# Kernel tuning notes

Measured on AMD Instinct MI355X. Metric: run time of the kernel, lower is better.

Reference implementation:

```python
import jax, jax.numpy as jnp
import numpy as np
from jax import lax

B, T1, T2, D, H = 4, 1024, 1024, 1024, 16
DK = D // H          # 64 per-head dim
K = 13               # conv kernel size
FF = 4 * D


def _ln(x, g, b, eps):
    mu = jnp.mean(x, axis=-1, keepdims=True)
    var = jnp.mean((x - mu) ** 2, axis=-1, keepdims=True)
    y = (x - mu) * lax.rsqrt(var + eps)
    if g is not None:
        y = y * g + b
    return y


def _conv1d(x, w, b):
    # x: (B, T, C) ; w: (O, C//H, K) grouped conv, 'same' padding
    y = lax.conv_general_dilated(
        x.transpose(0, 2, 1), w, window_strides=(1,),
        padding=[(K // 2, K // 2)],
        dimension_numbers=('NCH', 'OIH', 'NCH'),
        feature_group_count=H)
    return (y + b[None, :, None]).transpose(0, 2, 1)


def setup_inputs() -> dict:
    key = jax.random.key(0)
    ks = jax.random.split(key, 24)
    s = 0.02
    inp = {
        'noisy_feats': jax.random.normal(ks[0], (B, T1, D), jnp.float32),
        'clean_feats': jax.random.normal(ks[1], (B, T2, D), jnp.float32),
        't': jax.random.normal(ks[2], (B, D), jnp.float32),
        'ln_noisy_g': jnp.ones((D,), jnp.float32),
        'ln_noisy_b': jnp.zeros((D,), jnp.float32),
        'ln_clean_g': jnp.ones((D,), jnp.float32),
        'ln_clean_b': jnp.zeros((D,), jnp.float32),
        'ada_w': jax.random.normal(ks[3], (6 * D, D), jnp.float32) * s,
        'ada_b': jnp.zeros((6 * D,), jnp.float32),
        'wq': jax.random.normal(ks[4], (D, D // H, K), jnp.float32) * s,
        'bq': jnp.zeros((D,), jnp.float32),
        'wk': jax.random.normal(ks[5], (D, D // H, K), jnp.float32) * s,
        'bk': jnp.zeros((D,), jnp.float32),
        'wv': jax.random.normal(ks[6], (D, D // H, K), jnp.float32) * s,
        'bv': jnp.zeros((D,), jnp.float32),
        'fc_w': jax.random.normal(ks[7], (D, D), jnp.float32) * s,
        'fc_b': jnp.zeros((D,), jnp.float32),
        'ff_w1': jax.random.normal(ks[8], (FF, D), jnp.float32) * s,
        'ff_b1': jnp.zeros((FF,), jnp.float32),
        'ff_w2': jax.random.normal(ks[9], (D, FF), jnp.float32) * s,
        'ff_b2': jnp.zeros((D,), jnp.float32),
        'noisy_lengths': jax.random.randint(ks[10], (B,), 1, T1 + 1),
        'clean_lengths': jax.random.randint(ks[11], (B,), 1, T2 + 1),
    }
    return inp


def reference(noisy_feats, clean_feats, t,
              ln_noisy_g, ln_noisy_b, ln_clean_g, ln_clean_b,
              ada_w, ada_b, wq, bq, wk, bk, wv, bv, fc_w, fc_b,
              ff_w1, ff_b1, ff_w2, ff_b2,
              noisy_lengths, clean_lengths):
    # pre-norms (affine, eps=1e-5 torch default)
    noisy = _ln(noisy_feats, ln_noisy_g, ln_noisy_b, 1e-5)
    clean = _ln(clean_feats, ln_clean_g, ln_clean_b, 1e-5)

    # AdaLayerNormZero
    emb = jax.nn.silu(t) @ ada_w.T + ada_b                      # (B, 6D)
    shift_msa, scale_msa, gate_msa, shift_mlp, scale_mlp, gate_mlp = jnp.split(emb, 6, axis=1)
    normx = _ln(noisy, None, None, 1e-6) * (1.0 + scale_msa[:, None]) + shift_msa[:, None]

    # padding mask: True at pad positions (only context mask enters the scores)
    clean_mask = jnp.arange(T2)[None, :] >= clean_lengths[:, None]   # (B, T2)

    # grouped-conv QKV
    q = _conv1d(normx, wq, bq).reshape(B, T1, H, DK)
    k = _conv1d(clean, wk, bk).reshape(B, T2, H, DK)
    v = _conv1d(clean, wv, bv).reshape(B, T2, H, DK)

    scores = jnp.einsum('bqhd,bkhd->bhqk', q, k) / jnp.sqrt(jnp.float32(DK))
    scores = jnp.where(clean_mask[:, None, None, :], jnp.float32(-1e30), scores)
    p = jax.nn.softmax(scores, axis=-1)
    # rows where every key is masked -> zero (torch all_inf handling)
    all_masked = jnp.all(clean_mask, axis=-1)[:, None, None, None]
    p = jnp.where(all_masked, 0.0, p)

    out = jnp.einsum('bhqk,bkhd->bqhd', p, v).reshape(B, T1, D)
    out = out @ fc_w.T + fc_b

    x = noisy + gate_msa[:, None, :] * out
    n2 = _ln(x, None, None, 1e-6) * (1.0 + scale_mlp[:, None]) + shift_mlp[:, None]
    ff = jax.nn.gelu(n2 @ ff_w1.T + ff_b1, approximate=True) @ ff_w2.T + ff_b2
    return x + gate_mlp[:, None, :] * ff
```

## Files before the change

### kernel.cpp

```cpp
#include <hip/hip_runtime.h>
#include <hip/hip_bf16.h>

typedef __hip_bfloat16 bf16;
typedef __attribute__((ext_vector_type(8))) short short8;
typedef __attribute__((ext_vector_type(4))) float f32x4;

#define D_ 1024
#define SIXD 6144

__device__ __forceinline__ float bflo(unsigned int u){ union {unsigned int u; float f;} c; c.u = u << 16; return c.f; }
__device__ __forceinline__ float bfhi(unsigned int u){ union {unsigned int u; float f;} c; c.u = u & 0xFFFF0000u; return c.f; }
__device__ __forceinline__ float bload(const bf16* p){
  union {unsigned int u; float f;} c;
  c.u = ((unsigned int)(*reinterpret_cast<const unsigned short*>(p))) << 16;
  return c.f;
}
__device__ __forceinline__ bf16 bstore(float f){ return __float2bfloat16(f); }
__device__ __forceinline__ unsigned short bf16bits(float f){
  bf16 b = __float2bfloat16(f);
  return *reinterpret_cast<unsigned short*>(&b);
}

__device__ __forceinline__ void gload16(const bf16* g, bf16* l){
  __builtin_amdgcn_global_load_lds((const __attribute__((address_space(1))) unsigned int*)g,
                                   (__attribute__((address_space(3))) unsigned int*)l, 16, 0, 0);
}

__device__ __forceinline__ void pipe_sync(){
  asm volatile("s_waitcnt vmcnt(0)" ::: "memory");
  __builtin_amdgcn_s_barrier();
  __builtin_amdgcn_sched_barrier(0);
}

template<int ISBF>
__device__ __forceinline__ float ild(const void* p, size_t i){
  if (ISBF) return bload((const bf16*)p + i);
  return ((const float*)p)[i];
}

__device__ __forceinline__ float block_sum(float v, float* sh4){
  #pragma unroll
  for (int o = 32; o; o >>= 1) v += __shfl_down(v, o);
  __syncthreads();
  int lane = threadIdx.x & 63, wid = threadIdx.x >> 6;
  if (lane == 0) sh4[wid] = v;
  __syncthreads();
  return sh4[0] + sh4[1] + sh4[2] + sh4[3];
}

__global__ void detect_kernel(const unsigned int* g, int* flag){
  unsigned int u = *g;
  *flag = (u == 0x3F803F80u) ? 1 : 0;
}

template<int ISBF>
__device__ __forceinline__ void emb_body(const void* T, const void* AW, const void* AB,
                                         float* E, float* st){
  int b = blockIdx.y;
  int tid = threadIdx.x;
  for (int c = tid; c < D_; c += 256) {
    float x = ild<ISBF>(T, (size_t)b*D_ + c);
    st[c] = x / (1.f + expf(-x));
  }
  __syncthreads();
  int wid = tid >> 6, lane = tid & 63;
  int j = blockIdx.x * 4 + wid;
  float dot = 0.f;
  for (int c = lane; c < D_; c += 64) dot += ild<ISBF>(AW, (size_t)j*D_ + c) * st[c];
  #pragma unroll
  for (int o = 32; o; o >>= 1) dot += __shfl_down(dot, o);
  if (lane == 0) E[b*SIXD + j] = dot + ild<ISBF>(AB, j);
}
__global__ __launch_bounds__(256) void emb_kernel(const void* T, const void* AW, const void* AB,
                                                  const int* flagp, float* E){
  __shared__ float st[D_];
  if (*flagp) emb_body<1>(T, AW, AB, E, st); else emb_body<0>(T, AW, AB, E, st);
}

template<int ISBF>
__device__ __forceinline__ void ln_noisy_body(const void* X, const void* G, const void* Bt,
                                              const float* E, bf16* xbuf, bf16* normx, float* sh4){
  int r = blockIdx.x; int b = r >> 10;
  int tid = threadIdx.x; int c0 = tid * 4;
  size_t base = (size_t)r*D_ + c0;
  float f0 = ild<ISBF>(X, base+0), f1 = ild<ISBF>(X, base+1);
  float f2 = ild<ISBF>(X, base+2), f3 = ild<ISBF>(X, base+3);
  float mean = block_sum(f0+f1+f2+f3, sh4) * (1.f/D_);
  float var  = block_sum(f0*f0+f1*f1+f2*f2+f3*f3, sh4) * (1.f/D_) - mean*mean;
  float rstd = rsqrtf(fmaxf(var, 0.f) + 1e-5f);
  float y0 = (f0-mean)*rstd*ild<ISBF>(G,c0+0) + ild<ISBF>(Bt,c0+0);
  float y1 = (f1-mean)*rstd*ild<ISBF>(G,c0+1) + ild<ISBF>(Bt,c0+1);
  float y2 = (f2-mean)*rstd*ild<ISBF>(G,c0+2) + ild<ISBF>(Bt,c0+2);
  float y3 = (f3-mean)*rstd*ild<ISBF>(G,c0+3) + ild<ISBF>(Bt,c0+3);
  bf16* xo = xbuf + base;
  xo[0]=bstore(y0); xo[1]=bstore(y1); xo[2]=bstore(y2); xo[3]=bstore(y3);
  float m2 = block_sum(y0+y1+y2+y3, sh4) * (1.f/D_);
  float v2 = block_sum(y0*y0+y1*y1+y2*y2+y3*y3, sh4) * (1.f/D_) - m2*m2;
  float rstd2 = rsqrtf(fmaxf(v2, 0.f) + 1e-6f);
  const float* eb = E + b*SIXD;
  bf16* o = normx + base;
  o[0] = bstore((y0-m2)*rstd2*(1.f+eb[1024+c0+0]) + eb[c0+0]);
  o[1] = bstore((y1-m2)*rstd2*(1.f+eb[1024+c0+1]) + eb[c0+1]);
  o[2] = bstore((y2-m2)*rstd2*(1.f+eb[1024+c0+2]) + eb[c0+2]);
  o[3] = bstore((y3-m2)*rstd2*(1.f+eb[1024+c0+3]) + eb[c0+3]);
}
__global__ __launch_bounds__(256) void ln_noisy_fused(const void* X, const void* G, const void* Bt,
                                                      const float* E, bf16* xbuf, bf16* normx,
                                                      const int* flagp){
  __shared__ float sh4[4];
  if (*flagp) ln_noisy_body<1>(X,G,Bt,E,xbuf,normx,sh4); else ln_noisy_body<0>(X,G,Bt,E,xbuf,normx,sh4);
}

template<int ISBF>
__device__ __forceinline__ void ln_clean_body(const void* X, const void* G, const void* Bt,
                                              bf16* Y, float* sh4){
  int r = blockIdx.x;
  int tid = threadIdx.x; int c0 = tid * 4;
  size_t base = (size_t)r*D_ + c0;
  float f0 = ild<ISBF>(X, base+0), f1 = ild<ISBF>(X, base+1);
  float f2 = ild<ISBF>(X, base+2), f3 = ild<ISBF>(X, base+3);
  float mean = block_sum(f0+f1+f2+f3, sh4) * (1.f/D_);
  float var  = block_sum(f0*f0+f1*f1+f2*f2+f3*f3, sh4) * (1.f/D_) - mean*mean;
  float rstd = rsqrtf(fmaxf(var, 0.f) + 1e-5f);
  bf16* o = Y + base;
  o[0] = bstore((f0-mean)*rstd*ild<ISBF>(G,c0+0) + ild<ISBF>(Bt,c0+0));
  o[1] = bstore((f1-mean)*rstd*ild<ISBF>(G,c0+1) + ild<ISBF>(Bt,c0+1));
  o[2] = bstore((f2-mean)*rstd*ild<ISBF>(G,c0+2) + ild<ISBF>(Bt,c0+2));
  o[3] = bstore((f3-mean)*rstd*ild<ISBF>(G,c0+3) + ild<ISBF>(Bt,c0+3));
}
__global__ __launch_bounds__(256) void ln_clean_kernel(const void* X, const void* G, const void* Bt,
                                                       bf16* Y, const int* flagp){
  __shared__ float sh4[4];
  if (*flagp) ln_clean_body<1>(X,G,Bt,Y,sh4); else ln_clean_body<0>(X,G,Bt,Y,sh4);
}

__global__ __launch_bounds__(256) void ln2_kernel(const bf16* __restrict__ X, const float* __restrict__ E,
                                                  bf16* __restrict__ Y){
  __shared__ float sh4[4];
  int r = blockIdx.x; int b = r >> 10;
  int tid = threadIdx.x; int c0 = tid * 4;
  uint2 u = *reinterpret_cast<const uint2*>(X + (size_t)r*D_ + c0);
  float f0 = bflo(u.x), f1 = bfhi(u.x), f2 = bflo(u.y), f3 = bfhi(u.y);
  float mean = block_sum(f0+f1+f2+f3, sh4) * (1.f/D_);
  float var  = block_sum(f0*f0+f1*f1+f2*f2+f3*f3, sh4) * (1.f/D_) - mean*mean;
  float rstd = rsqrtf(fmaxf(var, 0.f) + 1e-6f);
  const float* eb = E + b*SIXD;
  bf16* o = Y + (size_t)r*D_ + c0;
  o[0] = bstore((f0-mean)*rstd*(1.f+eb[4096+c0+0]) + eb[3072+c0+0]);
  o[1] = bstore((f1-mean)*rstd*(1.f+eb[4096+c0+1]) + eb[3072+c0+1]);
  o[2] = bstore((f2-mean)*rstd*(1.f+eb[4096+c0+2]) + eb[3072+c0+2]);
  o[3] = bstore((f3-mean)*rstd*(1.f+eb[4096+c0+3]) + eb[3072+c0+3]);
}

template<int ISBF>
__device__ __forceinline__ void wtrans_body(const void* W, bf16* Wtr){
  size_t idx = (size_t)blockIdx.x * 256 + threadIdx.x;
  int si = idx & 63;
  size_t r = idx >> 6;
  int o = (int)(r & 63); r >>= 6;
  int k = (int)(r % 13);
  int g = (int)(r / 13);
  int i = si ^ ((o & 7) << 3);
  Wtr[idx] = bstore(ild<ISBF>(W, ((size_t)(g*64 + o)*64 + i)*13 + k));
}
__global__ __launch_bounds__(256) void conv_wtrans(const void* W, bf16* Wtr, const int* flagp){
  if (*flagp) wtrans_body<1>(W, Wtr); else wtrans_body<0>(W, Wtr);
}

template<int ISBF>
__device__ __forceinline__ void wconv_body(const void* W, bf16* o, int n){
  for (int i = blockIdx.x*256 + threadIdx.x; i < n; i += gridDim.x*256)
    o[i] = bstore(ild<ISBF>(W, (size_t)i));
}
__global__ __launch_bounds__(256) void wconv_kernel(const void* W, bf16* o, int n, const int* flagp){
  if (*flagp) wconv_body<1>(W, o, n); else wconv_body<0>(W, o, n);
}

template<int ISBF>
__device__ __forceinline__ void convl_body(const bf16* __restrict__ X,
                                           const bf16* __restrict__ Wtr, const void* Bias,
                                           bf16* __restrict__ Y,
                                           bf16* ws, bf16* xs){
  int tid = threadIdx.x;
  int wave = tid >> 6, lane = tid & 63;
  int fr = lane & 15, fq = lane >> 4;
  int t0 = blockIdx.x * 256;
  int g = blockIdx.y, b = blockIdx.z;
  const bf16* Wg = Wtr + (size_t)g*53248;
  #pragma unroll
  for (int p = 0; p < 13; ++p)
    gload16(Wg + ((size_t)p*512 + tid)*8, ws + (p*512 + tid)*8);
  const bf16* xg = X + ((size_t)b*1024)*D_ + g*64;
  for (int idx = tid; idx < 268*8; idx += 512) {
    int row = idx >> 3, q = idx & 7;
    int t = t0 - 6 + row;
    uint4 v = make_uint4(0,0,0,0);
    if (t >= 0 && t < 1024)
      v = *reinterpret_cast<const uint4*>(xg + (size_t)t*D_ + q*8);
    *reinterpret_cast<uint4*>(&xs[row*72 + q*8]) = v;
  }
  __syncthreads();
  f32x4 acc[2][4];
  #pragma unroll
  for (int i = 0; i < 2; ++i)
    #pragma unroll
    for (int j = 0; j < 4; ++j) acc[i][j] = (f32x4){0.f,0.f,0.f,0.f};
  int wrow = wave * 32;
  const bf16* a0 = xs + (wrow + fr)*72 + fq*8;
  for (int k = 0; k < 13; ++k) {
    const bf16* wk_ = ws + (k*64 + fr)*64;
    const bf16* ar = a0 + k*72;
    #pragma unroll
    for (int h = 0; h < 2; ++h) {
      int swz = (h*32 + fq*8) ^ ((fr & 7) << 3);
      short8 af0 = *reinterpret_cast<const short8*>(ar + h*32);
      short8 af1 = *reinterpret_cast<const short8*>(ar + 16*72 + h*32);
      #pragma unroll
      for (int tn = 0; tn < 4; ++tn) {
        short8 bv = *reinterpret_cast<const short8*>(wk_ + tn*1024 + swz);
        acc[0][tn] = __builtin_amdgcn_mfma_f32_16x16x32_bf16(af0, bv, acc[0][tn], 0,0,0);
        acc[1][tn] = __builtin_amdgcn_mfma_f32_16x16x32_bf16(af1, bv, acc[1][tn], 0,0,0);
      }
    }
  }
  #pragma unroll
  for (int tm = 0; tm < 2; ++tm) {
    #pragma unroll
    for (int tn = 0; tn < 4; ++tn) {
      int oc = g*64 + tn*16 + fr;
      float bb = ild<ISBF>(Bias, oc);
      #pragma unroll
      for (int r = 0; r < 4; ++r) {
        int tt = t0 + wrow + tm*16 + fq*4 + r;
        Y[((size_t)(b*1024 + tt))*D_ + oc] = bstore(acc[tm][tn][r] + bb);
      }
    }
  }
}
__global__ __launch_bounds__(512) void conv_lds(const bf16* X, const bf16* Wtr, const void* Bias,
                                                bf16* Y, const int* flagp){
  extern __shared__ bf16 smem[];
  bf16* ws = smem;
  bf16* xs = smem + 53248;
  if (*flagp) convl_body<1>(X, Wtr, Bias, Y, ws, xs);
  else        convl_body<0>(X, Wtr, Bias, Y, ws, xs);
}
#define CONV_LDS_BYTES ((53248 + 268*72) * 2)

__global__ __launch_bounds__(256) void attn_mfma(const bf16* __restrict__ Q, const bf16* __restrict__ Kb,
                                                 const bf16* __restrict__ V, const int* __restrict__ lens,
                                                 bf16* __restrict__ O){
  __shared__ bf16 qs[64*72];
  __shared__ bf16 ks[64*72];
  __shared__ bf16 vt[64*72];
  __shared__ bf16 ps[4][16*72];
  int tid = threadIdx.x;
  int wave = tid >> 6, lane = tid & 63;
  int fr = lane & 15, fq = lane >> 4;
  int qb = blockIdx.x, h = blockIdx.y, b = blockIdx.z;
  int len = lens[b]; len = len < 0 ? 0 : (len > 1024 ? 1024 : len);
  {
    int row = tid >> 2, col = (tid & 3) * 16;
    const bf16* src = Q + ((size_t)(b*1024 + qb*64 + row))*D_ + h*64 + col;
    *reinterpret_cast<uint4*>(&qs[row*72 + col])     = *reinterpret_cast<const uint4*>(src);
    *reinterpret_cast<uint4*>(&qs[row*72 + col + 8]) = *reinterpret_cast<const uint4*>(src + 8);
  }
  __syncthreads();
  short8 bq0 = *reinterpret_cast<const short8*>(&qs[(wave*16 + fr)*72 + fq*8]);
  short8 bq1 = *reinterpret_cast<const short8*>(&qs[(wave*16 + fr)*72 + 32 + fq*8]);
  f32x4 oacc[4];
  #pragma unroll
  for (int t = 0; t < 4; ++t) oacc[t] = (f32x4){0.f,0.f,0.f,0.f};
  float m_ = -1e30f, l_ = 0.f;
  int krow = tid >> 2, kcol = (tid & 3) * 16;
  int vk = (tid >> 3) * 2, vcol = (tid & 7) * 8;
  const bf16* kg = Kb + ((size_t)b*1024)*D_ + h*64;
  const bf16* vg = V  + ((size_t)b*1024)*D_ + h*64;
  for (int k0 = 0; k0 < len; k0 += 64) {
    uint4 kv0 = make_uint4(0,0,0,0), kv1 = make_uint4(0,0,0,0);
    uint4 va = make_uint4(0,0,0,0), vb = make_uint4(0,0,0,0);
    if (k0 + krow < len) {
      kv0 = *reinterpret_cast<const uint4*>(kg + (size_t)(k0+krow)*D_ + kcol);
      kv1 = *reinterpret_cast<const uint4*>(kg + (size_t)(k0+krow)*D_ + kcol + 8);
    }
    if (k0 + vk < len)     va = *reinterpret_cast<const uint4*>(vg + (size_t)(k0+vk)*D_ + vcol);
    if (k0 + vk + 1 < len) vb = *reinterpret_cast<const uint4*>(vg + (size_t)(k0+vk+1)*D_ + vcol);
    __syncthreads();
    *reinterpret_cast<uint4*>(&ks[krow*72 + kcol])     = kv0;
    *reinterpret_cast<uint4*>(&ks[krow*72 + kcol + 8]) = kv1;
    {
      union { uint4 u; unsigned short s[8]; } ca, cb; ca.u = va; cb.u = vb;
      #pragma unroll
      for (int j = 0; j < 8; ++j) {
        unsigned int w = ((unsigned int)cb.s[j] << 16) | (unsigned int)ca.s[j];
        int d = vcol + j;
        int blk = ((vk >> 3) ^ ((d >> 3) & 7)) << 3;
        *reinterpret_cast<unsigned int*>(&vt[d*72 + blk + (vk & 7)]) = w;
      }
    }
    __syncthreads();
    f32x4 s[4];
    #pragma unroll
    for (int f = 0; f < 4; ++f) {
      short8 ak0 = *reinterpret_cast<const short8*>(&ks[(f*16 + fr)*72 + fq*8]);
      short8 ak1 = *reinterpret_cast<const short8*>(&ks[(f*16 + fr)*72 + 32 + fq*8]);
      s[f] = (f32x4){0.f,0.f,0.f,0.f};
      s[f] = __builtin_amdgcn_mfma_f32_16x16x32_bf16(ak0, bq0, s[f], 0,0,0);
      s[f] = __builtin_amdgcn_mfma_f32_16x16x32_bf16(ak1, bq1, s[f], 0,0,0);
    }
    float p[4][4];
    float pmax = -1e30f;
    #pragma unroll
    for (int f = 0; f < 4; ++f)
      #pragma unroll
      for (int r = 0; r < 4; ++r) {
        float sv = (k0 + f*16 + fq*4 + r < len) ? s[f][r]*0.125f : -1e30f;
        p[f][r] = sv;
        pmax = fmaxf(pmax, sv);
      }
    pmax = fmaxf(pmax, __shfl_xor(pmax, 16));
    pmax = fmaxf(pmax, __shfl_xor(pmax, 32));
    float mnew = fmaxf(m_, pmax);
    float alpha = __expf(m_ - mnew);
    float psum = 0.f;
    #pragma unroll
    for (int f = 0; f < 4; ++f)
      #pragma unroll
      for (int r = 0; r < 4; ++r) {
        float pv = __expf(p[f][r] - mnew);
        p[f][r] = pv;
        psum += pv;
      }
    psum += __shfl_xor(psum, 16);
    psum += __shfl_xor(psum, 32);
    l_ = l_*alpha + psum;
    m_ = mnew;
    #pragma unroll
    for (int f = 0; f < 4; ++f) {
      unsigned int lo = ((unsigned int)bf16bits(p[f][1]) << 16) | (unsigned int)bf16bits(p[f][0]);
      unsigned int hi = ((unsigned int)bf16bits(p[f][3]) << 16) | (unsigned int)bf16bits(p[f][2]);
      unsigned int* pp = reinterpret_cast<unsigned int*>(&ps[wave][fr*72 + f*16 + fq*4]);
      pp[0] = lo; pp[1] = hi;
    }
    float aq[4];
    #pragma unroll
    for (int r = 0; r < 4; ++r) aq[r] = __shfl(alpha, fq*4 + r);
    #pragma unroll
    for (int tn = 0; tn < 4; ++tn)
      #pragma unroll
      for (int r = 0; r < 4; ++r) oacc[tn][r] *= aq[r];
    short8 ap0 = *reinterpret_cast<const short8*>(&ps[wave][fr*72 + fq*8]);
    short8 ap1 = *reinterpret_cast<const short8*>(&ps[wave][fr*72 + 32 + fq*8]);
    #pragma unroll
    for (int tn = 0; tn < 4; ++tn) {
      int d = tn*16 + fr;
      int sw = (d >> 3) & 7;
      short8 bv0 = *reinterpret_cast<const short8*>(&vt[d*72 + ((fq     ^ sw) << 3)]);
      short8 bv1 = *reinterpret_cast<const short8*>(&vt[d*72 + (((4+fq) ^ sw) << 3)]);
      oacc[tn] = __builtin_amdgcn_mfma_f32_16x16x32_bf16(ap0, bv0, oacc[tn], 0,0,0);
      oacc[tn] = __builtin_amdgcn_mfma_f32_16x16x32_bf16(ap1, bv1, oacc[tn], 0,0,0);
    }
  }
  float linv = (l_ > 0.f) ? 1.f/l_ : 0.f;
  float iq[4];
  #pragma unroll
  for (int r = 0; r < 4; ++r) iq[r] = __shfl(linv, fq*4 + r);
  #pragma unroll
  for (int r = 0; r < 4; ++r) {
    int q = qb*64 + wave*16 + fq*4 + r;
    bf16* op = O + ((size_t)(b*1024 + q))*D_ + h*64 + fr;
    #pragma unroll
    for (int tn = 0; tn < 4; ++tn)
      op[tn*16] = bstore(oacc[tn][r] * iq[r]);
  }
}

template<int ISBF>
__device__ __forceinline__ void mgemm_body(const bf16* __restrict__ A, const bf16* __restrict__ W,
                                           const void* bias, int bofs,
                                           int K, int ldA, int ldW, int Nst, int mode, int gate_ofs,
                                           bf16* xbuf, const float* emb, void* outb,
                                           bf16* As, bf16* Bs){
  int tid = threadIdx.x;
  int nwg = gridDim.x * gridDim.y;
  int flat = blockIdx.y * gridDim.x + blockIdx.x;
  int swz = (flat & 7) * (nwg >> 3) + (flat >> 3);
  int bx = swz % gridDim.x, by = swz / gridDim.x;
  int m0 = by * 128, n0 = bx * 128;
  int wave = tid >> 6, lane = tid & 63;
  int wr = wave >> 2, wc = wave & 3;
  int fr = lane & 15, fq = lane >> 4;
  int srow = tid >> 2, skc = (tid & 3) * 8;
  const bf16* Ag = A + (size_t)(m0 + srow)*ldA + skc;
  const bf16* Wg = W + (size_t)(n0 + srow)*ldW + skc;
  bf16* Asl = As + tid*8;
  bf16* Bsl = Bs + tid*8;
  const bf16* Afr = As + (wr*64 + fr)*32 + fq*8;
  const bf16* Bfr = Bs + (wc*32 + fr)*32 + fq*8;
  f32x4 acc[4][2];
  #pragma unroll
  for (int i = 0; i < 4; ++i)
    #pragma unroll
    for (int j = 0; j < 2; ++j) acc[i][j] = (f32x4){0.f,0.f,0.f,0.f};
  gload16(Ag,      Asl);
  gload16(Ag + 32, Asl + 4096);
  gload16(Wg,      Bsl);
  gload16(Wg + 32, Bsl + 4096);
  pipe_sync();
  int cur = 0;
  int nt = K >> 6;
  for (int t = 0; t < nt; ++t) {
    if (t + 1 < nt) {
      int k1 = (t + 1) << 6;
      int bo = (cur ^ 1) * 8192;
      gload16(Ag + k1,      Asl + bo);
      gload16(Ag + k1 + 32, Asl + bo + 4096);
      gload16(Wg + k1,      Bsl + bo);
      gload16(Wg + k1 + 32, Bsl + bo + 4096);
    }
    int co = cur * 8192;
    #pragma unroll
    for (int ks = 0; ks < 2; ++ks) {
      short8 af[4], bfv[2];
      #pragma unroll
      for (int tm = 0; tm < 4; ++tm) af[tm] = *reinterpret_cast<const short8*>(Afr + co + ks*4096 + tm*16*32);
      #pragma unroll
      for (int tn = 0; tn < 2; ++tn) bfv[tn] = *reinterpret_cast<const short8*>(Bfr + co + ks*4096 + tn*16*32);
      #pragma unroll
      for (int tm = 0; tm < 4; ++tm)
        #pragma unroll
        for (int tn = 0; tn < 2; ++tn)
          acc[tm][tn] = __builtin_amdgcn_mfma_f32_16x16x32_bf16(af[tm], bfv[tn], acc[tm][tn], 0, 0, 0);
    }
    if (t + 1 < nt) pipe_sync();
    cur ^= 1;
  }
  #pragma unroll
  for (int tm = 0; tm < 4; ++tm) {
    #pragma unroll
    for (int tn = 0; tn < 2; ++tn) {
      int nn = n0 + wc*32 + tn*16 + fr;
      float bv = bias ? ild<ISBF>(bias, (size_t)(bofs + nn)) : 0.f;
      #pragma unroll
      for (int r = 0; r < 4; ++r) {
        int mm = m0 + wr*64 + tm*16 + fq*4 + r;
        float v = acc[tm][tn][r] + bv;
        const float* eb = emb + (mm >> 10)*SIXD;
        if (mode == 1) {
          float tt = 0.7978845608028654f * (v + 0.044715f * v * v * v);
          ((bf16*)outb)[(size_t)mm*Nst + nn] = bstore(0.5f * v * (1.f + tanhf(tt)));
        } else if (mode == 2) {
          size_t xi = (size_t)mm*1024 + nn;
          xbuf[xi] = bstore(bload(xbuf + xi) + eb[gate_ofs + nn] * v);
        } else {
          size_t xi = (size_t)mm*1024 + nn;
          float rr = bload(xbuf + xi) + eb[gate_ofs + nn] * v;
          if (ISBF) ((bf16*)outb)[xi] = bstore(rr);
          else      ((float*)outb)[xi] = rr;
        }
      }
    }
  }
}
__global__ __launch_bounds__(512) void mgemm_kernel(const bf16* A, const bf16* W,
                                                    const void* bias, int bofs,
                                                    int K, int ldA, int ldW, int Nst, int mode, int gate_ofs,
                                                    bf16* xbuf, const float* emb, void* outb,
                                                    const int* flagp){
  __shared__ bf16 As[2*2*128*32];
  __shared__ bf16 Bs[2*2*128*32];
  if (*flagp) mgemm_body<1>(A,W,bias,bofs,K,ldA,ldW,Nst,mode,gate_ofs,xbuf,emb,outb,As,Bs);
  else        mgemm_body<0>(A,W,bias,bofs,K,ldA,ldW,Nst,mode,gate_ofs,xbuf,emb,outb,As,Bs);
}

extern "C" void kernel_launch(void* const* d_in, const int* in_sizes, int n_in,
                              void* d_out, int out_size, void* d_ws, size_t ws_size,
                              hipStream_t stream) {
  (void)in_sizes; (void)n_in; (void)out_size; (void)ws_size;
  const void* noisy = d_in[0];
  const void* clean = d_in[1];
  const void* t     = d_in[2];
  const void* lng   = d_in[3];
  const void* lnb   = d_in[4];
  const void* lcg   = d_in[5];
  const void* lcb   = d_in[6];
  const void* ada_w = d_in[7];
  const void* ada_b = d_in[8];
  const void* wq    = d_in[9];
  const void* bq    = d_in[10];
  const void* wk    = d_in[11];
  const void* bk    = d_in[12];
  const void* wv    = d_in[13];
  const void* bv    = d_in[14];
  const void* fc_w  = d_in[15];
  const void* fc_b  = d_in[16];
  const void* ff_w1 = d_in[17];
  const void* ff_b1 = d_in[18];
  const void* ff_w2 = d_in[19];
  const void* ff_b2 = d_in[20];
  const int*  clen  = (const int*)d_in[22];

  char* w = (char*)d_ws;
  int*   flagp = (int*)w;
  float* embp  = (float*)(w + 4096);
  bf16*  xbuf  = (bf16*)(w + 102400);
  bf16*  normx = (bf16*)(w + 8491008);
  bf16*  cleanb= (bf16*)(w + 16879616);
  bf16*  qb    = (bf16*)(w + 25268224);
  bf16*  kbuf  = (bf16*)(w + 33656832);
  bf16*  vbuf  = (bf16*)(w + 42045440);
  bf16*  wqtr  = (bf16*)(w + 50434048);
  bf16*  wktr  = (bf16*)(w + 52137984);
  bf16*  wvtr  = (bf16*)(w + 53841920);
  bf16*  ff1h  = qb;
  bf16*  attno = cleanb;
  bf16*  n2b   = normx;
  bf16*  fc_wb = wqtr;
  bf16*  ffw1b = vbuf;
  bf16*  ffw2b = cleanb;

  detect_kernel<<<1, 1, 0, stream>>>((const unsigned int*)lng, flagp);
  emb_kernel<<<dim3(1536, 4), 256, 0, stream>>>(t, ada_w, ada_b, flagp, embp);
  ln_noisy_fused<<<4096, 256, 0, stream>>>(noisy, lng, lnb, embp, xbuf, normx, flagp);
  ln_clean_kernel<<<4096, 256, 0, stream>>>(clean, lcg, lcb, cleanb, flagp);
  conv_wtrans<<<3328, 256, 0, stream>>>(wq, wqtr, flagp);
  conv_wtrans<<<3328, 256, 0, stream>>>(wk, wktr, flagp);
  conv_wtrans<<<3328, 256, 0, stream>>>(wv, wvtr, flagp);
  conv_lds<<<dim3(4, 16, 4), 512, CONV_LDS_BYTES, stream>>>(normx,  wqtr, bq, qb,   flagp);
  conv_lds<<<dim3(4, 16, 4), 512, CONV_LDS_BYTES, stream>>>(cleanb, wktr, bk, kbuf, flagp);
  conv_lds<<<dim3(4, 16, 4), 512, CONV_LDS_BYTES, stream>>>(cleanb, wvtr, bv, vbuf, flagp);
  wconv_kernel<<<1024, 256, 0, stream>>>(fc_w, fc_wb, 1048576, flagp);
  attn_mfma<<<dim3(16, 16, 4), 256, 0, stream>>>(qb, kbuf, vbuf, clen, attno);
  wconv_kernel<<<2048, 256, 0, stream>>>(ff_w1, ffw1b, 4194304, flagp);
  mgemm_kernel<<<dim3(8, 32), 512, 0, stream>>>(attno, fc_wb, fc_b, 0,
                                                1024, 1024, 1024, 1024, 2, 2048, xbuf, embp, nullptr, flagp);
  wconv_kernel<<<2048, 256, 0, stream>>>(ff_w2, ffw2b, 4194304, flagp);
  ln2_kernel<<<4096, 256, 0, stream>>>(xbuf, embp, n2b);
  mgemm_kernel<<<dim3(16, 32), 512, 0, stream>>>(n2b, ffw1b, ff_b1, 0,
                                                 1024, 1024, 1024, 2048, 1, 0, xbuf, embp, ff1h, flagp);
  mgemm_kernel<<<dim3(8, 32), 512, 0, stream>>>(ff1h, ffw2b, ff_b2, 0,
                                                2048, 2048, 4096, 1024, 2, 5120, xbuf, embp, nullptr, flagp);
  mgemm_kernel<<<dim3(16, 32), 512, 0, stream>>>(n2b, ffw1b + (size_t)2048*1024, ff_b1, 2048,
                                                 1024, 1024, 1024, 2048, 1, 0, xbuf, embp, ff1h, flagp);
  mgemm_kernel<<<dim3(8, 32), 512, 0, stream>>>(ff1h, ffw2b + 2048, nullptr, 0,
                                                2048, 2048, 4096, 1024, 3, 5120, xbuf, embp, d_out, flagp);
}
```

Measured before the change: 472.3 us.

## Deepen GEMM global-to-LDS pipeline to four stages with prefetch distance two

The MFMA GEMM's shared-memory staging grows from two buffers to a four-slot ring, and tiles are now prefetched two K-steps ahead. Each iteration uses a partial vmcnt wait and a single barrier, replacing the full drain-and-barrier at the end of every step. The goal is to hide more global-load latency behind MFMA work. In exchange, LDS use doubles to 128KB of dynamic shared memory per block, which lowers the number of resident blocks per CU and depends on the runtime allowing that much dynamic LDS.

```diff
diff --git a/kernel.cpp b/kernel.cpp
--- a/kernel.cpp
+++ b/kernel.cpp
@@ -24,12 +24,6 @@
 __device__ __forceinline__ void gload16(const bf16* g, bf16* l){
   __builtin_amdgcn_global_load_lds((const __attribute__((address_space(1))) unsigned int*)g,
                                    (__attribute__((address_space(3))) unsigned int*)l, 16, 0, 0);
-}
-
-__device__ __forceinline__ void pipe_sync(){
-  asm volatile("s_waitcnt vmcnt(0)" ::: "memory");
-  __builtin_amdgcn_s_barrier();
-  __builtin_amdgcn_sched_barrier(0);
 }
 
 template<int ISBF>
@@ -402,23 +396,33 @@
   for (int i = 0; i < 4; ++i)
     #pragma unroll
     for (int j = 0; j < 2; ++j) acc[i][j] = (f32x4){0.f,0.f,0.f,0.f};
-  gload16(Ag,      Asl);
-  gload16(Ag + 32, Asl + 4096);
-  gload16(Wg,      Bsl);
-  gload16(Wg + 32, Bsl + 4096);
-  pipe_sync();
-  int cur = 0;
   int nt = K >> 6;
+  gload16(Ag,       Asl);
+  gload16(Ag + 32,  Asl + 4096);
+  gload16(Wg,       Bsl);
+  gload16(Wg + 32,  Bsl + 4096);
+  gload16(Ag + 64,  Asl + 8192);
+  gload16(Ag + 96,  Asl + 8192 + 4096);
+  gload16(Wg + 64,  Bsl + 8192);
+  gload16(Wg + 96,  Bsl + 8192 + 4096);
   for (int t = 0; t < nt; ++t) {
-    if (t + 1 < nt) {
-      int k1 = (t + 1) << 6;
-      int bo = (cur ^ 1) * 8192;
-      gload16(Ag + k1,      Asl + bo);
-      gload16(Ag + k1 + 32, Asl + bo + 4096);
-      gload16(Wg + k1,      Bsl + bo);
-      gload16(Wg + k1 + 32, Bsl + bo + 4096);
-    }
-    int co = cur * 8192;
+    if (t + 2 < nt) {
+      int k2 = (t + 2) << 6;
+      int bo = ((t + 2) & 3) * 8192;
+      gload16(Ag + k2,      Asl + bo);
+      gload16(Ag + k2 + 32, Asl + bo + 4096);
+      gload16(Wg + k2,      Bsl + bo);
+      gload16(Wg + k2 + 32, Bsl + bo + 4096);
+      asm volatile("s_waitcnt vmcnt(8)" ::: "memory");
+    } else if (t + 1 < nt) {
+      asm volatile("s_waitcnt vmcnt(4)" ::: "memory");
+    } else {
+      asm volatile("s_waitcnt vmcnt(0)" ::: "memory");
+    }
+    __builtin_amdgcn_sched_barrier(0);
+    __builtin_amdgcn_s_barrier();
+    __builtin_amdgcn_sched_barrier(0);
+    int co = (t & 3) * 8192;
     #pragma unroll
     for (int ks = 0; ks < 2; ++ks) {
       short8 af[4], bfv[2];
@@ -432,8 +436,6 @@
         for (int tn = 0; tn < 2; ++tn)
           acc[tm][tn] = __builtin_amdgcn_mfma_f32_16x16x32_bf16(af[tm], bfv[tn], acc[tm][tn], 0, 0, 0);
     }
-    if (t + 1 < nt) pipe_sync();
-    cur ^= 1;
   }
   #pragma unroll
   for (int tm = 0; tm < 4; ++tm) {
@@ -467,11 +469,13 @@
                                                     int K, int ldA, int ldW, int Nst, int mode, int gate_ofs,
                                                     bf16* xbuf, const float* emb, void* outb,
                                                     const int* flagp){
-  __shared__ bf16 As[2*2*128*32];
-  __shared__ bf16 Bs[2*2*128*32];
+  extern __shared__ bf16 gsm[];
+  bf16* As = gsm;
+  bf16* Bs = gsm + 32768;
   if (*flagp) mgemm_body<1>(A,W,bias,bofs,K,ldA,ldW,Nst,mode,gate_ofs,xbuf,emb,outb,As,Bs);
   else        mgemm_body<0>(A,W,bias,bofs,K,ldA,ldW,Nst,mode,gate_ofs,xbuf,emb,outb,As,Bs);
 }
+#define MGEMM_LDS_BYTES (65536 * 2)
 
 extern "C" void kernel_launch(void* const* d_in, const int* in_sizes, int n_in,
                               void* d_out, int out_size, void* d_ws, size_t ws_size,
@@ -532,16 +536,16 @@
   wconv_kernel<<<1024, 256, 0, stream>>>(fc_w, fc_wb, 1048576, flagp);
   attn_mfma<<<dim3(16, 16, 4), 256, 0, stream>>>(qb, kbuf, vbuf, clen, attno);
   wconv_kernel<<<2048, 256, 0, stream>>>(ff_w1, ffw1b, 4194304, flagp);
-  mgemm_kernel<<<dim3(8, 32), 512, 0, stream>>>(attno, fc_wb, fc_b, 0,
+  mgemm_kernel<<<dim3(8, 32), 512, MGEMM_LDS_BYTES, stream>>>(attno, fc_wb, fc_b, 0,
                                                 1024, 1024, 1024, 1024, 2, 2048, xbuf, embp, nullptr, flagp);
   wconv_kernel<<<2048, 256, 0, stream>>>(ff_w2, ffw2b, 4194304, flagp);
   ln2_kernel<<<4096, 256, 0, stream>>>(xbuf, embp, n2b);
-  mgemm_kernel<<<dim3(16, 32), 512, 0, stream>>>(n2b, ffw1b, ff_b1, 0,
+  mgemm_kernel<<<dim3(16, 32), 512, MGEMM_LDS_BYTES, stream>>>(n2b, ffw1b, ff_b1, 0,
                                                  1024, 1024, 1024, 2048, 1, 0, xbuf, embp, ff1h, flagp);
-  mgemm_kernel<<<dim3(8, 32), 512, 0, stream>>>(ff1h, ffw2b, ff_b2, 0,
+  mgemm_kernel<<<dim3(8, 32), 512, MGEMM_LDS_BYTES, stream>>>(ff1h, ffw2b, ff_b2, 0,
                                                 2048, 2048, 4096, 1024, 2, 5120, xbuf, embp, nullptr, flagp);
-  mgemm_kernel<<<dim3(16, 32), 512, 0, stream>>>(n2b, ffw1b + (size_t)2048*1024, ff_b1, 2048,
+  mgemm_kernel<<<dim3(16, 32), 512, MGEMM_LDS_BYTES, stream>>>(n2b, ffw1b + (size_t)2048*1024, ff_b1, 2048,
                                                  1024, 1024, 1024, 2048, 1, 0, xbuf, embp, ff1h, flagp);
-  mgemm_kernel<<<dim3(8, 32), 512, 0, stream>>>(ff1h, ffw2b + 2048, nullptr, 0,
+  mgemm_kernel<<<dim3(8, 32), 512, MGEMM_LDS_BYTES, stream>>>(ff1h, ffw2b + 2048, nullptr, 0,
                                                 2048, 2048, 4096, 1024, 3, 5120, xbuf, embp, d_out, flagp);
 }
```

Measured after the change: 461.7 us. -2.2%, faster.
